# Optimization experiments

Measured on AMD Instinct MI355X. Metric: run time of the kernel, lower is better.

Reference implementation:

```python
import jax, jax.numpy as jnp
import numpy as np

KS = 3
N = KS * KS
LN_EPS = 1e-5


def conv2d(x, w, stride=1, pad=0):
    return jax.lax.conv_general_dilated(
        x, w, (stride, stride), [(pad, pad), (pad, pad)],
        dimension_numbers=('NCHW', 'OIHW', 'NCHW'))


def layer_norm(x, g, b):
    mu = jnp.mean(x, axis=-1, keepdims=True)
    var = jnp.mean(jnp.square(x - mu), axis=-1, keepdims=True)
    return (x - mu) * jax.lax.rsqrt(var + LN_EPS) * g + b


def l2norm(x):
    n = jnp.sqrt(jnp.sum(jnp.square(x), axis=-1, keepdims=True))
    return x / jnp.maximum(n, 1e-12)


def deform_conv(x, w_p, b_p, w_d):
    # canonical DeformConv2d (kernel 3, pad 1, stride 1, no modulation)
    B, C, H, W = x.shape
    off = conv2d(x, w_p, stride=1, pad=1) + b_p[None, :, None, None]  # [B,2N,H,W]
    xp = jnp.pad(x, ((0, 0), (0, 0), (1, 1), (1, 1)))
    Hp, Wp = H + 2, W + 2
    pn = jnp.stack(jnp.meshgrid(jnp.arange(-1, 2), jnp.arange(-1, 2), indexing='ij'), 0)
    pn = pn.reshape(2, N).astype(x.dtype)  # kernel offsets, row-major (dx,dy)
    p0x = jnp.arange(1, H + 1, dtype=x.dtype)
    p0y = jnp.arange(1, W + 1, dtype=x.dtype)
    # sampling coords, [B,H,W,N]
    px = off[:, :N].transpose(0, 2, 3, 1) + p0x[None, :, None, None] + pn[0][None, None, None, :]
    py = off[:, N:].transpose(0, 2, 3, 1) + p0y[None, None, :, None] + pn[1][None, None, None, :]
    fx = jnp.floor(px)
    fy = jnp.floor(py)
    qlx = jnp.clip(fx, 0, Hp - 1)
    qly = jnp.clip(fy, 0, Wp - 1)
    qrx = jnp.clip(fx + 1, 0, Hp - 1)
    qry = jnp.clip(fy + 1, 0, Wp - 1)
    pxc = jnp.clip(px, 0, Hp - 1)
    pyc = jnp.clip(py, 0, Wp - 1)
    g_lt = (1 + (qlx - pxc)) * (1 + (qly - pyc))
    g_rb = (1 - (qrx - pxc)) * (1 - (qry - pyc))
    g_lb = (1 + (qlx - pxc)) * (1 - (qry - pyc))
    g_rt = (1 - (qrx - pxc)) * (1 + (qly - pyc))
    xf = xp.reshape(B, C, Hp * Wp)

    def gat(ix, iy):
        idx = (ix.astype(jnp.int32) * Wp + iy.astype(jnp.int32)).reshape(B, 1, -1)
        g = jnp.take_along_axis(xf, jnp.broadcast_to(idx, (B, C, idx.shape[-1])), axis=2)
        return g.reshape(B, C, H, W, N)

    xo = (g_lt[:, None] * gat(qlx, qly) + g_rb[:, None] * gat(qrx, qry)
          + g_lb[:, None] * gat(qlx, qry) + g_rt[:, None] * gat(qrx, qly))
    # [B,C,H,W,N] -> [B,C,H*ks,W*ks] (row = h*ks+kr, col = w*ks+kc)
    xo = xo.reshape(B, C, H, W, KS, KS).transpose(0, 1, 2, 4, 3, 5).reshape(B, C, H * KS, W * KS)
    return conv2d(xo, w_d, stride=KS, pad=0)


def setup_inputs() -> dict:
    key = jax.random.key(0)
    ks = jax.random.split(key, 8)
    B, C, H, W, heads = 4, 192, 64, 64, 6
    hid = 4 * C
    return {
        'x': jax.random.normal(ks[0], (B, C, H, W), dtype=jnp.float32),
        'gamma1': jnp.ones((C,), jnp.float32),
        'beta1': jnp.zeros((C,), jnp.float32),
        'gamma2': jnp.ones((C,), jnp.float32),
        'beta2': jnp.zeros((C,), jnp.float32),
        'temperature': jnp.ones((heads, 1, 1), jnp.float32),
        'w_qkv': jax.random.normal(ks[1], (3 * C, C), jnp.float32) * 0.02,
        'w_proj': jax.random.normal(ks[2], (C, C), jnp.float32) * 0.02,
        'w_p': jax.random.normal(ks[3], (2 * N, C, KS, KS), jnp.float32) * 0.01,
        'b_p': jnp.zeros((2 * N,), jnp.float32),
        'w_d': jax.random.normal(ks[4], (C, C, KS, KS), jnp.float32) * 0.02,
        'w_fc1': jax.random.normal(ks[5], (C, hid), jnp.float32) * 0.02,
        'b_fc1': jnp.zeros((hid,), jnp.float32),
        'w_fc2': jax.random.normal(ks[6], (hid, C), jnp.float32) * 0.02,
        'b_fc2': jnp.zeros((C,), jnp.float32),
    }


def reference(x, gamma1, beta1, gamma2, beta2, temperature, w_qkv, w_proj,
              w_p, b_p, w_d, w_fc1, b_fc1, w_fc2, b_fc2):
    B, C, H, W = x.shape
    heads = temperature.shape[0]
    xs = x.reshape(B, C, H * W).transpose(0, 2, 1)  # [B,HW,C]
    shortcut = xs
    xn = layer_norm(xs, gamma1, beta1).transpose(0, 2, 1).reshape(B, C, H, W)
    # SSA: deformable-conv query + channel attention over C
    q = deform_conv(xn, w_p, b_p, w_d)
    qkv = jnp.einsum('bchw,oc->bohw', xn, w_qkv)
    k_spe, v_spe = qkv[:, C:2 * C], qkv[:, 2 * C:]

    def split(t):
        return t.reshape(B, heads, C // heads, H * W)

    qh = split(q)
    kh = l2norm(split(k_spe))
    vh = l2norm(split(v_spe))
    attn = jnp.einsum('bhcn,bhdn->bhcd', qh, kh) * temperature[None]
    attn = jax.nn.softmax(attn, axis=-1)
    out = jnp.einsum('bhcd,bhdn->bhcn', attn, vh).reshape(B, C, H, W)
    out = jnp.einsum('bchw,oc->bohw', out, w_proj)
    xs2 = shortcut + out.reshape(B, C, H * W).transpose(0, 2, 1)
    h1 = layer_norm(xs2, gamma2, beta2)
    m = jax.nn.gelu(h1 @ w_fc1 + b_fc1, approximate=False) @ w_fc2 + b_fc2
    xs3 = xs2 + m
    return xs3.transpose(0, 2, 1).reshape(B, C, H, W)
```

## Files before the change

kernel.cpp:

```cpp
#include <hip/hip_runtime.h>
#include <math.h>

typedef unsigned short u16;
typedef unsigned int u32;
typedef short s16x8 __attribute__((ext_vector_type(8)));
typedef float f32x4 __attribute__((ext_vector_type(4)));

#define AS1 __attribute__((address_space(1)))
#define AS3 __attribute__((address_space(3)))

__device__ __forceinline__ float bf2f(u16 u) {
    union { u32 i; float f; } v; v.i = ((u32)u) << 16; return v.f;
}
__device__ __forceinline__ u16 f2bf(float f) {
    union { float f; u32 i; } v; v.f = f;
    u32 r = v.i + 0x7fffu + ((v.i >> 16) & 1u);
    return (u16)(r >> 16);
}
__device__ __forceinline__ void gll16(const u16* g, u16* l) {
    __builtin_amdgcn_global_load_lds((const AS1 u32*)g, (AS3 u32*)l, 16, 0, 0);
}

__global__ void prep_kernel(const float* __restrict__ wd, const float* __restrict__ wqkv,
                            const float* __restrict__ wfc1, const float* __restrict__ wfc2,
                            const float* __restrict__ wp,
                            u16* __restrict__ wdT, u16* __restrict__ wkvT,
                            u16* __restrict__ wf1T, u16* __restrict__ wf2T,
                            u16* __restrict__ wpT)
{
    int i = blockIdx.x * 256 + threadIdx.x;
    if (i < 331776) {
        int o = i / 1728, r = i % 1728;
        int p = r / 192, c = r % 192;
        wdT[i] = f2bf(wd[(o * 192 + c) * 9 + p]);
    }
    if (i < 73728) {
        int o = i / 192, c = i % 192;
        wkvT[i] = f2bf(wqkv[(192 + o) * 192 + c]);
    }
    if (i < 147456) {
        int n = i / 192, c = i % 192;
        wf1T[i] = f2bf(wfc1[c * 768 + n]);
        int n2 = i / 768, hh = i % 768;
        wf2T[i] = f2bf(wfc2[hh * 192 + n2]);
    }
    if (i < 31104) {
        int n = i / 1728, r = i % 1728;
        int p = r / 192, c = r % 192;
        wpT[i] = f2bf(wp[(n * 192 + c) * 9 + p]);
    } else if (i < 55296) {
        wpT[i] = 0;
    }
}

__global__ __launch_bounds__(256) void ln1_kernel(const float* __restrict__ x,
                                                  const float* __restrict__ g,
                                                  const float* __restrict__ be,
                                                  u16* __restrict__ xn)
{
    __shared__ float red0[256], red1[256];
    __shared__ float mu_s[64], rs_s[64];
    __shared__ u16 tile[64 * 194];
    int t = threadIdx.x, tl = t & 63, cg = t >> 6;
    int m0 = blockIdx.x * 64;
    int b = m0 >> 12, hw0 = m0 & 4095;
    const float* xb = x + (size_t)b * 786432 + hw0 + tl;
    float s = 0.f, s2 = 0.f;
    for (int cc = cg; cc < 192; cc += 4) { float v = xb[cc * 4096]; s += v; s2 += v * v; }
    red0[t] = s; red1[t] = s2;
    __syncthreads();
    if (t < 64) {
        float a = red0[t] + red0[64 + t] + red0[128 + t] + red0[192 + t];
        float q = red1[t] + red1[64 + t] + red1[128 + t] + red1[192 + t];
        float mu = a * (1.f / 192.f);
        float var = q * (1.f / 192.f) - mu * mu;
        mu_s[t] = mu; rs_s[t] = rsqrtf(var + 1e-5f);
    }
    __syncthreads();
    float mu = mu_s[tl], rs = rs_s[tl];
    for (int cc = cg; cc < 192; cc += 4) {
        float v = (xb[cc * 4096] - mu) * rs * g[cc] + be[cc];
        tile[tl * 194 + cc] = f2bf(v);
    }
    __syncthreads();
    u32* dst = (u32*)(xn + (size_t)m0 * 192);
    for (int i = t; i < 64 * 96; i += 256) {
        int r = i / 96, c2 = i % 96;
        dst[i] = *(const u32*)&tile[r * 194 + c2 * 2];
    }
}

__global__ __launch_bounds__(256) void offconv_kernel(const u16* __restrict__ xn,
                                                      const u16* __restrict__ wpT,
                                                      const float* __restrict__ bp,
                                                      float* __restrict__ off)
{
    __shared__ u16 As[64 * 200];
    __shared__ u16 Bs[32 * 200];
    int bh = blockIdx.x;
    int b = bh >> 6, h = bh & 63;
    int t = threadIdx.x;
    int lane = t & 63, wv = t >> 6;
    f32x4 acc[2];
#pragma unroll
    for (int j = 0; j < 2; j++) { acc[j][0] = 0.f; acc[j][1] = 0.f; acc[j][2] = 0.f; acc[j][3] = 0.f; }
    int r = t >> 2, cq = (t & 3) * 48;
    for (int p = 0; p < 9; p++) {
        int dh = p / 3 - 1, dw = p % 3 - 1;
        int hr = h + dh, wr = r + dw;
        bool valid = (hr >= 0) && (hr < 64) && (wr >= 0) && (wr < 64);
        const u16* src = xn + ((size_t)(b * 4096 + hr * 64 + wr)) * 192 + cq;
#pragma unroll
        for (int j = 0; j < 6; j++) {
            s16x8 v = {0, 0, 0, 0, 0, 0, 0, 0};
            if (valid) v = *(const s16x8*)(src + j * 8);
            *(s16x8*)&As[r * 200 + cq + j * 8] = v;
        }
#pragma unroll
        for (int i = 0; i < 3; i++) {
            int q = t + i * 256;
            int n = q / 24, c8 = q % 24;
            *(s16x8*)&Bs[n * 200 + c8 * 8] =
                *(const s16x8*)(wpT + n * 1728 + p * 192 + c8 * 8);
        }
        __syncthreads();
#pragma unroll
        for (int kc = 0; kc < 6; kc++) {
            s16x8 af = *(const s16x8*)&As[(wv * 16 + (lane & 15)) * 200 + kc * 32 + (lane >> 4) * 8];
            s16x8 b0 = *(const s16x8*)&Bs[(lane & 15) * 200 + kc * 32 + (lane >> 4) * 8];
            s16x8 b1 = *(const s16x8*)&Bs[(16 + (lane & 15)) * 200 + kc * 32 + (lane >> 4) * 8];
            acc[0] = __builtin_amdgcn_mfma_f32_16x16x32_bf16(af, b0, acc[0], 0, 0, 0);
            acc[1] = __builtin_amdgcn_mfma_f32_16x16x32_bf16(af, b1, acc[1], 0, 0, 0);
        }
        __syncthreads();
    }
    int col = lane & 15;
    int wbase = wv * 16 + (lane >> 4) * 4;
#pragma unroll
    for (int j = 0; j < 2; j++) {
        int n = j * 16 + col;
        if (n < 18) {
            float bb = bp[n];
#pragma unroll
            for (int rr = 0; rr < 4; rr++) {
                int w = wbase + rr;
                off[((size_t)(b * 4096 + h * 64 + w)) * 18 + n] = acc[j][rr] + bb;
            }
        }
    }
}

__global__ __launch_bounds__(256) void gemm_deform(const u16* __restrict__ xn,
                                                   const float* __restrict__ off,
                                                   const u16* __restrict__ wdT,
                                                   u16* __restrict__ qt)
{
    __shared__ u16 As[32 * 200];
    __shared__ u16 Bs[192 * 32];
    __shared__ int sidx[32][9][4];
    __shared__ float swt[32][9][4];
    int t = threadIdx.x, lane = t & 63, wv = t >> 6;
    int m0 = blockIdx.x * 32;
    int b = m0 >> 12;
    for (int i = t; i < 288; i += 256) {
        int mi = i / 9, p = i % 9;
        int m = m0 + mi;
        int hw = m & 4095;
        int h = hw >> 6, w = hw & 63;
        float ox = off[(size_t)m * 18 + p];
        float oy = off[(size_t)m * 18 + 9 + p];
        float px = ox + (float)(h + 1) + (float)(p / 3 - 1);
        float py = oy + (float)(w + 1) + (float)(p % 3 - 1);
        float fx = floorf(px), fy = floorf(py);
        float qlx = fminf(fmaxf(fx, 0.f), 65.f);
        float qly = fminf(fmaxf(fy, 0.f), 65.f);
        float qrx = fminf(fmaxf(fx + 1.f, 0.f), 65.f);
        float qry = fminf(fmaxf(fy + 1.f, 0.f), 65.f);
        float pxc = fminf(fmaxf(px, 0.f), 65.f);
        float pyc = fminf(fmaxf(py, 0.f), 65.f);
        float gxl = 1.f + (qlx - pxc), gxr = 1.f - (qrx - pxc);
        float gyl = 1.f + (qly - pyc), gyr = 1.f - (qry - pyc);
        int xl = (int)qlx, xr = (int)qrx, yl = (int)qly, yr = (int)qry;
        int cx[4] = {xl, xr, xl, xr};
        int cy[4] = {yl, yr, yr, yl};
        float cw[4] = {gxl * gyl, gxr * gyr, gxl * gyr, gxr * gyl};
#pragma unroll
        for (int k = 0; k < 4; k++) {
            bool ok = (cx[k] >= 1) && (cx[k] <= 64) && (cy[k] >= 1) && (cy[k] <= 64);
            sidx[mi][p][k] = ok ? (b * 4096 + (cx[k] - 1) * 64 + (cy[k] - 1)) * 192 : 0;
            swt[mi][p][k] = ok ? cw[k] : 0.f;
        }
    }
    __syncthreads();
    f32x4 acc[2][3];
#pragma unroll
    for (int i = 0; i < 2; i++)
#pragma unroll
        for (int j = 0; j < 3; j++) {
            acc[i][j][0] = 0.f; acc[i][j][1] = 0.f; acc[i][j][2] = 0.f; acc[i][j][3] = 0.f;
        }
    for (int p = 0; p < 9; p++) {
        for (int i = t; i < 768; i += 256) {
            int mi = i / 24, ch = (i % 24) * 8;
            const int*   si = sidx[mi][p];
            const float* sw = swt[mi][p];
            float v[8] = {0.f, 0.f, 0.f, 0.f, 0.f, 0.f, 0.f, 0.f};
#pragma unroll
            for (int k = 0; k < 4; k++) {
                s16x8 cv = *(const s16x8*)(xn + si[k] + ch);
                float wt = sw[k];
#pragma unroll
                for (int j = 0; j < 8; j++) v[j] += wt * bf2f((u16)cv[j]);
            }
            s16x8 ov;
#pragma unroll
            for (int j = 0; j < 8; j++) ov[j] = (short)f2bf(v[j]);
            *(s16x8*)&As[mi * 200 + ch] = ov;
        }
        for (int kk = 0; kk < 6; kk++) {
#pragma unroll 1
            for (int j = wv; j < 12; j += 4)
                gll16(wdT + (size_t)(j * 16 + (lane >> 2)) * 1728 + p * 192 + kk * 32 + (lane & 3) * 8,
                      Bs + j * 512);
            asm volatile("s_waitcnt vmcnt(0)" ::: "memory");
            __syncthreads();
            s16x8 af[2], bfr[3];
#pragma unroll
            for (int i = 0; i < 2; i++)
                af[i] = *(const s16x8*)&As[(i * 16 + (lane & 15)) * 200 + kk * 32 + (lane >> 4) * 8];
#pragma unroll
            for (int j = 0; j < 3; j++)
                bfr[j] = *(const s16x8*)&Bs[(wv * 48 + j * 16 + (lane & 15)) * 32 + (lane >> 4) * 8];
#pragma unroll
            for (int i = 0; i < 2; i++)
#pragma unroll
                for (int j = 0; j < 3; j++)
                    acc[i][j] = __builtin_amdgcn_mfma_f32_16x16x32_bf16(af[i], bfr[j], acc[i][j], 0, 0, 0);
            __syncthreads();
        }
    }
    int col = lane & 15;
#pragma unroll
    for (int i = 0; i < 2; i++)
#pragma unroll
        for (int j = 0; j < 3; j++) {
            int mm = m0 + i * 16 + (lane >> 4) * 4;
            int nn = wv * 48 + j * 16 + col;
#pragma unroll
            for (int r = 0; r < 4; r++)
                qt[(size_t)(mm + r) * 192 + nn] = f2bf(acc[i][j][r]);
        }
}

template<int BM, int BN, int WM, int WN, int EP>
__global__ __launch_bounds__((BM / WM) * (BN / WN) * 64)
void gemm_bt(const u16* __restrict__ A, int lda,
             const u16* __restrict__ B, int ldb, int bstride,
             void* __restrict__ out, int ldc,
             const float* __restrict__ ex1, int K)
{
    constexpr int BK = 32;
    constexpr int WAVES_M = BM / WM, WAVES_N = BN / WN, NW = WAVES_M * WAVES_N;
    constexpr int TM = WM / 16, TN = WN / 16;
    constexpr int NLA = BM / 16, NLB = BN / 16;
    __shared__ u16 As[BM * BK];
    __shared__ u16 Bs[BN * BK];
    int tid = threadIdx.x;
    int lane = tid & 63, wv = tid >> 6;
    int wm = wv % WAVES_M, wn = wv / WAVES_M;
    int m0 = blockIdx.x * BM, n0 = blockIdx.y * BN;
    const u16* Bp = B + (size_t)(m0 >> 12) * bstride;
    f32x4 acc[TM][TN];
#pragma unroll
    for (int i = 0; i < TM; i++)
#pragma unroll
        for (int j = 0; j < TN; j++) {
            acc[i][j][0] = 0.f; acc[i][j][1] = 0.f; acc[i][j][2] = 0.f; acc[i][j][3] = 0.f;
        }
    int arow_l = lane >> 2;
    int acol_l = (lane & 3) * 8;
    for (int k0 = 0; k0 < K; k0 += BK) {
#pragma unroll 1
        for (int j = wv; j < NLA + NLB; j += NW) {
            if (j < NLA) {
                int row = j * 16 + arow_l;
                gll16(A + (size_t)(m0 + row) * lda + k0 + acol_l, As + j * 512);
            } else {
                int row = (j - NLA) * 16 + arow_l;
                gll16(Bp + (size_t)(n0 + row) * ldb + k0 + acol_l, Bs + (j - NLA) * 512);
            }
        }
        asm volatile("s_waitcnt vmcnt(0)" ::: "memory");
        __syncthreads();
        s16x8 af[TM], bfr[TN];
#pragma unroll
        for (int i = 0; i < TM; i++)
            af[i] = *(const s16x8*)&As[(wm * WM + i * 16 + (lane & 15)) * BK + (lane >> 4) * 8];
#pragma unroll
        for (int j = 0; j < TN; j++)
            bfr[j] = *(const s16x8*)&Bs[(wn * WN + j * 16 + (lane & 15)) * BK + (lane >> 4) * 8];
#pragma unroll
        for (int i = 0; i < TM; i++)
#pragma unroll
            for (int j = 0; j < TN; j++)
                acc[i][j] = __builtin_amdgcn_mfma_f32_16x16x32_bf16(af[i], bfr[j], acc[i][j], 0, 0, 0);
        __syncthreads();
    }
    int col = lane & 15;
#pragma unroll
    for (int i = 0; i < TM; i++)
#pragma unroll
        for (int j = 0; j < TN; j++) {
            int mm = m0 + wm * WM + i * 16 + (lane >> 4) * 4;
            int nn = n0 + wn * WN + j * 16 + col;
            if (EP == 0) {
                u16* o = (u16*)out;
#pragma unroll
                for (int r = 0; r < 4; r++) o[(size_t)(mm + r) * ldc + nn] = f2bf(acc[i][j][r]);
            } else if (EP == 1) {
                float* o = (float*)out;
                const float* xr = ex1 + (size_t)(mm >> 12) * 786432 + (size_t)nn * 4096 + (mm & 4095);
#pragma unroll
                for (int r = 0; r < 4; r++) o[(size_t)(mm + r) * ldc + nn] = acc[i][j][r] + xr[r];
            } else if (EP == 2) {
                u16* o = (u16*)out;
                float bb = ex1[nn];
#pragma unroll
                for (int r = 0; r < 4; r++) {
                    float v = acc[i][j][r] + bb;
                    o[(size_t)(mm + r) * ldc + nn] = f2bf(0.5f * v * (1.f + erff(v * 0.70710678118654752f)));
                }
            } else {
                float* o = (float*)out;
                float bb = ex1[nn];
#pragma unroll
                for (int r = 0; r < 4; r++) o[(size_t)(mm + r) * ldc + nn] = acc[i][j][r] + bb;
            }
        }
}

__global__ __launch_bounds__(384) void norm_kernel(const u16* __restrict__ kv,
                                                   float* __restrict__ norm2)
{
    int b = blockIdx.y, ch = blockIdx.x;
    int t = threadIdx.x;
    const u16* base = kv + ((size_t)(b * 4096 + ch * 128)) * 384 + t;
    float s = 0.f;
    for (int r = 0; r < 128; r++) { float v = bf2f(base[(size_t)r * 384]); s += v * v; }
    atomicAdd(&norm2[b * 384 + t], s);
}

__global__ __launch_bounds__(64) void attnp_kernel(const u16* __restrict__ qt,
                                                   const u16* __restrict__ kvt,
                                                   float* __restrict__ raw)
{
    __shared__ float qT[32 * 69];
    __shared__ float kT[32 * 69];
    int ch = blockIdx.x, h = blockIdx.y, b = blockIdx.z;
    int t = threadIdx.x;
    size_t base = (size_t)(b * 4096 + ch * 64);
    for (int e = t; e < 2048; e += 64) {
        int r = e >> 5, c = e & 31;
        qT[c * 69 + r] = bf2f(qt[(base + r) * 192 + h * 32 + c]);
        kT[c * 69 + r] = bf2f(kvt[(base + r) * 384 + h * 32 + c]);
    }
    __syncthreads();
    int tc = t >> 3, td = t & 7;
    int c0 = tc * 4, d0 = td * 4;
    float acc[4][4] = {};
    for (int r = 0; r < 64; r++) {
        float qv[4], kv4[4];
#pragma unroll
        for (int u = 0; u < 4; u++) { qv[u] = qT[(c0 + u) * 69 + r]; kv4[u] = kT[(d0 + u) * 69 + r]; }
#pragma unroll
        for (int u = 0; u < 4; u++)
#pragma unroll
            for (int v = 0; v < 4; v++) acc[u][v] += qv[u] * kv4[v];
    }
    float* dst = raw + ((size_t)(b * 6 + h)) * 1024;
#pragma unroll
    for (int u = 0; u < 4; u++)
#pragma unroll
        for (int v = 0; v < 4; v++)
            atomicAdd(&dst[(c0 + u) * 32 + d0 + v], acc[u][v]);
}

__global__ __launch_bounds__(1024) void softmax_kernel(const float* __restrict__ raw,
                                                       const float* __restrict__ norm2,
                                                       const float* __restrict__ temp,
                                                       float* __restrict__ att2)
{
    int h = blockIdx.x, b = blockIdx.y;
    int t = threadIdx.x;
    int c = t >> 5, d = t & 31;
    __shared__ float invk[32], invv[32];
    if (t < 32)       invk[t] = 1.f / fmaxf(sqrtf(norm2[b * 384 + h * 32 + t]), 1e-12f);
    else if (t < 64)  invv[t - 32] = 1.f / fmaxf(sqrtf(norm2[b * 384 + 192 + h * 32 + (t - 32)]), 1e-12f);
    __syncthreads();
    float T = temp[h];
    float v = raw[((size_t)(b * 6 + h) * 32 + c) * 32 + d] * invk[d] * T;
    float mx = v;
    for (int s = 16; s > 0; s >>= 1) mx = fmaxf(mx, __shfl_xor(mx, s, 32));
    float e = expf(v - mx);
    float sm = e;
    for (int s = 16; s > 0; s >>= 1) sm += __shfl_xor(sm, s, 32);
    att2[((size_t)(b * 6 + h) * 32 + c) * 32 + d] = (e / sm) * invv[d];
}

__global__ __launch_bounds__(192) void mb_kernel(const float* __restrict__ wproj,
                                                 const float* __restrict__ att2,
                                                 u16* __restrict__ Mb)
{
    int o2 = blockIdx.x, b = blockIdx.y, t = threadIdx.x;
    int h = t >> 5, d = t & 31;
    float s = 0.f;
#pragma unroll
    for (int c = 0; c < 32; c++)
        s += wproj[o2 * 192 + h * 32 + c] * att2[((size_t)(b * 6 + h) * 32 + c) * 32 + d];
    Mb[((size_t)b * 192 + o2) * 192 + t] = f2bf(s);
}

__global__ __launch_bounds__(256) void ln2_kernel(const float* __restrict__ xs2,
                                                  const float* __restrict__ g,
                                                  const float* __restrict__ be,
                                                  u16* __restrict__ h1)
{
    int t = threadIdx.x;
    int wv = t >> 6, l = t & 63;
    size_t m = (size_t)blockIdx.x * 4 + wv;
    const float* row = xs2 + m * 192;
    float v0 = row[l], v1 = row[l + 64], v2 = row[l + 128];
    float s = v0 + v1 + v2, s2 = v0 * v0 + v1 * v1 + v2 * v2;
    for (int sh = 32; sh > 0; sh >>= 1) { s += __shfl_xor(s, sh); s2 += __shfl_xor(s2, sh); }
    float mu = s * (1.f / 192.f);
    float var = s2 * (1.f / 192.f) - mu * mu;
    float rs = rsqrtf(var + 1e-5f);
    u16* o = h1 + m * 192;
    o[l]       = f2bf((v0 - mu) * rs * g[l]       + be[l]);
    o[l + 64]  = f2bf((v1 - mu) * rs * g[l + 64]  + be[l + 64]);
    o[l + 128] = f2bf((v2 - mu) * rs * g[l + 128] + be[l + 128]);
}

__global__ __launch_bounds__(256) void final_kernel(const float* __restrict__ xs2,
                                                    const float* __restrict__ m2,
                                                    float* __restrict__ out)
{
    __shared__ float tile[192 * 65];
    int blk = blockIdx.x;
    int b = blk >> 6, hw0 = (blk & 63) * 64;
    int t = threadIdx.x;
    size_t mbase = ((size_t)b * 4096 + hw0) * 192;
    for (int i = t; i < 64 * 192; i += 256) {
        int r = i / 192, c = i % 192;
        tile[c * 65 + r] = xs2[mbase + i] + m2[mbase + i];
    }
    __syncthreads();
    for (int i = t; i < 64 * 192; i += 256) {
        int c = i / 64, r = i % 64;
        out[(size_t)b * 786432 + (size_t)c * 4096 + hw0 + r] = tile[c * 65 + r];
    }
}

extern "C" void kernel_launch(void* const* d_in, const int* in_sizes, int n_in,
                              void* d_out, int out_size, void* d_ws, size_t ws_size,
                              hipStream_t stream)
{
    const float* x      = (const float*)d_in[0];
    const float* gamma1 = (const float*)d_in[1];
    const float* beta1  = (const float*)d_in[2];
    const float* gamma2 = (const float*)d_in[3];
    const float* beta2  = (const float*)d_in[4];
    const float* temp   = (const float*)d_in[5];
    const float* w_qkv  = (const float*)d_in[6];
    const float* w_proj = (const float*)d_in[7];
    const float* w_p    = (const float*)d_in[8];
    const float* b_p    = (const float*)d_in[9];
    const float* w_d    = (const float*)d_in[10];
    const float* w_fc1  = (const float*)d_in[11];
    const float* b_fc1  = (const float*)d_in[12];
    const float* w_fc2  = (const float*)d_in[13];
    const float* b_fc2  = (const float*)d_in[14];
    float* out = (float*)d_out;
    char* ws = (char*)d_ws;

    u16*   xn    = (u16*)(ws + 0);
    float* off   = (float*)(ws + 6291456);
    u16*   adef  = (u16*)(ws + 7471104);
    u16*   wpT   = adef;
    u16*   m1    = adef;
    float* m2    = (float*)(ws + 7471104 + 25165824);
    u16*   qt    = (u16*)(ws + 64094208);
    u16*   kvt   = (u16*)(ws + 70385664);
    float* norm2 = (float*)(ws + 82968576);
    float* araw  = (float*)(ws + 82974720);
    float* att2  = (float*)(ws + 83073024);
    u16*   Mb    = (u16*)(ws + 83171328);
    float* xs2   = (float*)(ws + 83318784);
    u16*   h1    = xn;
    u16*   wdT   = (u16*)(ws + 95901696);
    u16*   wkvT  = (u16*)(ws + 96565248);
    u16*   wf1T  = (u16*)(ws + 96712704);
    u16*   wf2T  = (u16*)(ws + 97007616);

    hipMemsetAsync(norm2, 0, 6144 + 98304, stream);
    prep_kernel<<<1296, 256, 0, stream>>>(w_d, w_qkv, w_fc1, w_fc2, w_p, wdT, wkvT, wf1T, wf2T, wpT);
    ln1_kernel<<<256, 256, 0, stream>>>(x, gamma1, beta1, xn);
    offconv_kernel<<<256, 256, 0, stream>>>(xn, wpT, b_p, off);
    gemm_deform<<<512, 256, 0, stream>>>(xn, off, wdT, qt);
    gemm_bt<128, 128, 64, 64, 0><<<dim3(128, 3), 256, 0, stream>>>(xn, 192, wkvT, 192, 0, kvt, 384, nullptr, 192);
    norm_kernel<<<dim3(32, 4), 384, 0, stream>>>(kvt, norm2);
    attnp_kernel<<<dim3(64, 6, 4), 64, 0, stream>>>(qt, kvt, araw);
    softmax_kernel<<<dim3(6, 4), 1024, 0, stream>>>(araw, norm2, temp, att2);
    mb_kernel<<<dim3(192, 4), 192, 0, stream>>>(w_proj, att2, Mb);
    gemm_bt<32, 192, 32, 96, 1><<<dim3(512, 1), 128, 0, stream>>>(kvt + 192, 384, Mb, 192, 192 * 192, xs2, 192, x, 192);
    ln2_kernel<<<4096, 256, 0, stream>>>(xs2, gamma2, beta2, h1);
    gemm_bt<128, 128, 64, 64, 2><<<dim3(128, 6), 256, 0, stream>>>(h1, 192, wf1T, 192, 0, m1, 768, b_fc1, 192);
    gemm_bt<32, 192, 32, 96, 3><<<dim3(512, 1), 128, 0, stream>>>(m1, 768, wf2T, 768, 0, m2, 192, b_fc2, 768);
    final_kernel<<<256, 256, 0, stream>>>(xs2, m2, out);
}
```

Measured before the change: 293.4 us.

## Double-buffer deform gather and load weight fragments directly from global

The deform-conv GEMM now double-buffers the bilinearly sampled A tile in shared memory. Gather loads for the next kernel tap are issued before the MFMA loop on the current tap, so their latency overlaps compute. The B-operand staging through LDS via global_load_lds is removed, and each wave reads its weight fragments straight from global memory, which drops the per-k-step waitcnt and two barriers. This uses more registers for the prefetched gathers, and the weight reads are now uncoalesced global loads that depend on cache hits.

```diff
diff --git a/kernel.cpp b/kernel.cpp
--- a/kernel.cpp
+++ b/kernel.cpp
@@ -155,8 +155,7 @@
                                                    const u16* __restrict__ wdT,
                                                    u16* __restrict__ qt)
 {
-    __shared__ u16 As[32 * 200];
-    __shared__ u16 Bs[192 * 32];
+    __shared__ u16 As[2][32 * 200];
     __shared__ int sidx[32][9][4];
     __shared__ float swt[32][9][4];
     int t = threadIdx.x, lane = t & 63, wv = t >> 6;
@@ -199,43 +198,79 @@
         for (int j = 0; j < 3; j++) {
             acc[i][j][0] = 0.f; acc[i][j][1] = 0.f; acc[i][j][2] = 0.f; acc[i][j][3] = 0.f;
         }
-    for (int p = 0; p < 9; p++) {
-        for (int i = t; i < 768; i += 256) {
-            int mi = i / 24, ch = (i % 24) * 8;
-            const int*   si = sidx[mi][p];
-            const float* sw = swt[mi][p];
+    int mi_[3], ch_[3];
+#pragma unroll
+    for (int u = 0; u < 3; u++) { int c = t + u * 256; mi_[u] = c / 24; ch_[u] = (c % 24) * 8; }
+
+    {
+        s16x8 pc[3][4];
+#pragma unroll
+        for (int u = 0; u < 3; u++) {
+            const int* si = sidx[mi_[u]][0];
+#pragma unroll
+            for (int k = 0; k < 4; k++) pc[u][k] = *(const s16x8*)(xn + si[k] + ch_[u]);
+        }
+#pragma unroll
+        for (int u = 0; u < 3; u++) {
+            const float* sw = swt[mi_[u]][0];
             float v[8] = {0.f, 0.f, 0.f, 0.f, 0.f, 0.f, 0.f, 0.f};
 #pragma unroll
             for (int k = 0; k < 4; k++) {
-                s16x8 cv = *(const s16x8*)(xn + si[k] + ch);
                 float wt = sw[k];
 #pragma unroll
-                for (int j = 0; j < 8; j++) v[j] += wt * bf2f((u16)cv[j]);
+                for (int j = 0; j < 8; j++) v[j] += wt * bf2f((u16)pc[u][k][j]);
             }
             s16x8 ov;
 #pragma unroll
             for (int j = 0; j < 8; j++) ov[j] = (short)f2bf(v[j]);
-            *(s16x8*)&As[mi * 200 + ch] = ov;
-        }
+            *(s16x8*)&As[0][mi_[u] * 200 + ch_[u]] = ov;
+        }
+    }
+    __syncthreads();
+
+    for (int p = 0; p < 9; p++) {
+        int cur = p & 1;
+        s16x8 nc[3][4];
+        if (p < 8) {
+#pragma unroll
+            for (int u = 0; u < 3; u++) {
+                const int* si = sidx[mi_[u]][p + 1];
+#pragma unroll
+                for (int k = 0; k < 4; k++) nc[u][k] = *(const s16x8*)(xn + si[k] + ch_[u]);
+            }
+        }
+        const u16* wp_base = wdT + p * 192;
+#pragma unroll
         for (int kk = 0; kk < 6; kk++) {
-#pragma unroll 1
-            for (int j = wv; j < 12; j += 4)
-                gll16(wdT + (size_t)(j * 16 + (lane >> 2)) * 1728 + p * 192 + kk * 32 + (lane & 3) * 8,
-                      Bs + j * 512);
-            asm volatile("s_waitcnt vmcnt(0)" ::: "memory");
-            __syncthreads();
             s16x8 af[2], bfr[3];
 #pragma unroll
             for (int i = 0; i < 2; i++)
-                af[i] = *(const s16x8*)&As[(i * 16 + (lane & 15)) * 200 + kk * 32 + (lane >> 4) * 8];
+                af[i] = *(const s16x8*)&As[cur][(i * 16 + (lane & 15)) * 200 + kk * 32 + (lane >> 4) * 8];
 #pragma unroll
             for (int j = 0; j < 3; j++)
-                bfr[j] = *(const s16x8*)&Bs[(wv * 48 + j * 16 + (lane & 15)) * 32 + (lane >> 4) * 8];
+                bfr[j] = *(const s16x8*)(wp_base + (size_t)(wv * 48 + j * 16 + (lane & 15)) * 1728 + kk * 32 + (lane >> 4) * 8);
 #pragma unroll
             for (int i = 0; i < 2; i++)
 #pragma unroll
                 for (int j = 0; j < 3; j++)
                     acc[i][j] = __builtin_amdgcn_mfma_f32_16x16x32_bf16(af[i], bfr[j], acc[i][j], 0, 0, 0);
+        }
+        if (p < 8) {
+#pragma unroll
+            for (int u = 0; u < 3; u++) {
+                const float* sw = swt[mi_[u]][p + 1];
+                float v[8] = {0.f, 0.f, 0.f, 0.f, 0.f, 0.f, 0.f, 0.f};
+#pragma unroll
+                for (int k = 0; k < 4; k++) {
+                    float wt = sw[k];
+#pragma unroll
+                    for (int j = 0; j < 8; j++) v[j] += wt * bf2f((u16)nc[u][k][j]);
+                }
+                s16x8 ov;
+#pragma unroll
+                for (int j = 0; j < 8; j++) ov[j] = (short)f2bf(v[j]);
+                *(s16x8*)&As[cur ^ 1][mi_[u] * 200 + ch_[u]] = ov;
+            }
             __syncthreads();
         }
     }
```

Result: no change. 292.4 us (-0.3%).
